# Optimization experiments

Measured on AMD Instinct MI355X. Metric: run time of the kernel, lower is better.

Reference implementation:

```python
import jax, jax.numpy as jnp
import numpy as np

B, N, M, F = 64, 2048, 2048, 4   # batch, n_pred_points, n_gt_points, feature cols
D = 2                            # loss_indices = [0, 1] -> (x, y) coords


def setup_inputs() -> dict:
    key = jax.random.key(0)
    k1, k2 = jax.random.split(key)
    preds = jax.random.normal(k1, (B, N, F), dtype=jnp.float32)
    targs = jax.random.normal(k2, (B, M, F), dtype=jnp.float32)
    subcoef = jnp.ones((D,), dtype=jnp.float32)
    return {"preds": preds, "targs": targs, "subcoef": subcoef}


def _bidirectional_nn_loss(p, t, subcoef):
    # p: [B, N, D] pred coords, t: [B, M, D] gt coords
    # squared euclidean pairwise distances [B, N, M]
    d2 = (jnp.sum(p * p, axis=-1)[:, :, None]
          + jnp.sum(t * t, axis=-1)[:, None, :]
          - 2.0 * jnp.einsum('bnd,bmd->bnm', p, t))
    # gt_tree: nearest gt for every pred point
    nn_gt = jnp.argmin(d2, axis=2)    # [B, N]
    # pred_tree: nearest pred for every gt point
    nn_pr = jnp.argmin(d2, axis=1)    # [B, M]
    t_nn = jnp.take_along_axis(t, nn_gt[:, :, None], axis=1)  # [B, N, D]
    p_nn = jnp.take_along_axis(p, nn_pr[:, :, None], axis=1)  # [B, M, D]
    move_preds_to_gt = jnp.sum(jnp.abs(p - t_nn) * subcoef)   # subcoef only on this term
    move_gts_to_pred = jnp.sum(jnp.abs(p_nn - t))
    return move_preds_to_gt + move_gts_to_pred


def reference(preds, targs, subcoef):
    p = preds[..., :D]   # loss_indices = [0, 1]
    t = targs[..., :D]
    return _bidirectional_nn_loss(p, t, subcoef)
```

## Files before the change

kernel.cpp:

```cpp
#include <hip/hip_runtime.h>

constexpr int B = 64;
constexpr int NQ = 2048;
constexpr int M = 2048;
constexpr int F = 4;
constexpr int BLOCK = 256;
constexpr int P = 8;
constexpr int CHUNK = 16;
constexpr int NCHUNK = M / CHUNK;
constexpr unsigned DMASK = 0xFFFFFF80u;
constexpr float BIAS = 64.0f;
constexpr int QTOT = 2 * B * NQ;
constexpr int QHALF = QTOT / 2;

typedef float v2f __attribute__((ext_vector_type(2)));

__device__ __forceinline__ unsigned fbits(float x) {
    union { float f; unsigned u; } c; c.f = x; return c.u;
}
__device__ __forceinline__ float min3f(float a, float b, float c) {
    float r;
    asm("v_min3_f32 %0, %1, %2, %3" : "=v"(r) : "v"(a), "v"(b), "v"(c));
    return r;
}

template <int S>
__global__ void __launch_bounds__(BLOCK)
nn_scan(const float* __restrict__ preds,
        const float* __restrict__ targs,
        unsigned* __restrict__ keys,
        float* __restrict__ out) {
    constexpr int CPB = NCHUNK / S;
    __shared__ float4 sxy[CPB * 8];
    __shared__ float2 snm[CPB * 8];

    const int s   = blockIdx.x;
    const int b   = blockIdx.y;
    const int dir = blockIdx.z;
    const int tid = threadIdx.x;

    if (s == 0 && b == 0 && dir == 0 && tid == 0) *out = 0.0f;

    const float* qsrc = dir ? targs : preds;
    const float* csrc = dir ? preds : targs;

    const float* cb_ = csrc + ((size_t)b * M + (size_t)s * CPB * CHUNK) * F;
    for (int g = tid; g < CPB * 8; g += BLOCK) {
        const float4 a = *reinterpret_cast<const float4*>(cb_ + (size_t)(2 * g) * F);
        const float4 c = *reinterpret_cast<const float4*>(cb_ + (size_t)(2 * g + 1) * F);
        sxy[g] = make_float4(a.x, c.x, a.y, c.y);
        snm[g] = make_float2(fmaf(a.y, a.y, a.x * a.x) + BIAS,
                             fmaf(c.y, c.y, c.x * c.x) + BIAS);
    }
    __syncthreads();

    float ax[P], ay[P];
    unsigned bkey[P];
    #pragma unroll
    for (int j = 0; j < P; ++j) {
        const int n = j * BLOCK + tid;
        const float2 p = *reinterpret_cast<const float2*>(qsrc + ((size_t)b * NQ + n) * F);
        ax[j] = -2.0f * p.x;
        ay[j] = -2.0f * p.y;
        bkey[j] = 0xFFFFFFFFu;
    }

    #pragma unroll 2
    for (int c = 0; c < CPB; ++c) {
        float cbm[P];
        #pragma unroll
        for (int j = 0; j < P; ++j) cbm[j] = 3.4028235e38f;
        #pragma unroll
        for (int i = 0; i < 8; ++i) {
            const float4 q  = sxy[c * 8 + i];
            const float2 nn = snm[c * 8 + i];
            #pragma unroll
            for (int j = 0; j < P; ++j) {
                const float d0 = fmaf(ax[j], q.x, fmaf(ay[j], q.z, nn.x));
                const float d1 = fmaf(ax[j], q.y, fmaf(ay[j], q.w, nn.y));
                cbm[j] = min3f(d0, d1, cbm[j]);
            }
        }
        const unsigned gc = (unsigned)(s * CPB + c);
        #pragma unroll
        for (int j = 0; j < P; ++j) {
            const unsigned key = (fbits(cbm[j]) & DMASK) | gc;
            bkey[j] = key < bkey[j] ? key : bkey[j];
        }
    }

    unsigned* kout = keys + (size_t)s * QTOT + ((size_t)dir * B + b) * NQ;
    #pragma unroll
    for (int j = 0; j < P; ++j) kout[j * BLOCK + tid] = bkey[j];
}

template <int S>
__global__ void __launch_bounds__(BLOCK)
nn_combine(const float* __restrict__ preds,
           const float* __restrict__ targs,
           const float* __restrict__ subcoef,
           const unsigned* __restrict__ keys,
           float* __restrict__ out) {
    __shared__ float wsum[BLOCK / 64];
    const int q0 = blockIdx.x * BLOCK + threadIdx.x;
    const int b  = q0 >> 11;
    const int n  = q0 & 2047;

    const float c0 = subcoef[0], c1 = subcoef[1];
    float acc = 0.0f;

    #pragma unroll
    for (int dir = 0; dir < 2; ++dir) {
        const int qid = q0 + dir * QHALF;
        const float* qsrc = dir ? targs : preds;
        const float* csrc = dir ? preds : targs;
        const float2 p = *reinterpret_cast<const float2*>(qsrc + ((size_t)b * NQ + n) * F);
        const float ax = -2.0f * p.x, ay = -2.0f * p.y;

        unsigned k = 0xFFFFFFFFu;
        #pragma unroll
        for (int s = 0; s < S; ++s) {
            const unsigned ks = keys[(size_t)s * QTOT + qid];
            k = ks < k ? ks : k;
        }
        const int cwin = (int)(k & 0x7Fu);
        const unsigned dbits = k & DMASK;

        const float4* cand = reinterpret_cast<const float4*>(
            csrc + ((size_t)b * M + (size_t)cwin * CHUNK) * F);
        float qx = 0.0f, qy = 0.0f;
        int found = 0;
        #pragma unroll
        for (int i = 0; i < CHUNK; ++i) {
            const float4 t4 = cand[i];
            const float x = t4.x, y = t4.y;
            const float nrm = fmaf(y, y, x * x) + BIAS;
            const float d = fmaf(ax, x, fmaf(ay, y, nrm));
            const bool hit = (((fbits(d) & DMASK) == dbits) && !found);
            qx = hit ? x : qx;
            qy = hit ? y : qy;
            found = hit ? 1 : found;
        }
        if (!found) { qx = cand[0].x; qy = cand[0].y; }

        const float w0 = dir ? 1.0f : c0;
        const float w1 = dir ? 1.0f : c1;
        acc += fabsf(p.x - qx) * w0 + fabsf(p.y - qy) * w1;
    }

    #pragma unroll
    for (int off = 32; off > 0; off >>= 1) acc += __shfl_down(acc, off, 64);
    if ((threadIdx.x & 63) == 0) wsum[threadIdx.x >> 6] = acc;
    __syncthreads();
    if (threadIdx.x == 0) {
        float ssum = 0.0f;
        #pragma unroll
        for (int w = 0; w < BLOCK / 64; ++w) ssum += wsum[w];
        atomicAdd(out, ssum);
    }
}

constexpr int PF = 2;
constexpr int CH_F4 = 9;
__global__ void __launch_bounds__(BLOCK)
nn_fallback(const float* __restrict__ preds,
            const float* __restrict__ targs,
            const float* __restrict__ subcoef,
            float* __restrict__ out) {
    __shared__ float4 sc4[NCHUNK * CH_F4];
    __shared__ float  wsum[BLOCK / 64];
    const int dir = blockIdx.z, b = blockIdx.y, tid = threadIdx.x;
    const float* src = dir ? targs : preds;
    const float* dst = dir ? preds : targs;
    const float* dstb = dst + (size_t)b * M * F;
    for (int g = tid; g < M / 2; g += BLOCK) {
        const float4 a = *reinterpret_cast<const float4*>(dstb + (size_t)(2 * g) * F);
        const float4 c = *reinterpret_cast<const float4*>(dstb + (size_t)(2 * g + 1) * F);
        sc4[(g >> 3) * CH_F4 + (g & 7)] = make_float4(a.x, c.x, a.y, c.y);
    }
    __syncthreads();
    const int base = blockIdx.x * (BLOCK * PF);
    float px[PF], py[PF], axr[PF], ayr[PF];
    unsigned bkey[PF];
    #pragma unroll
    for (int j = 0; j < PF; ++j) {
        const int n = base + j * BLOCK + tid;
        const float2 p = *reinterpret_cast<const float2*>(src + ((size_t)b * NQ + n) * F);
        px[j] = p.x; py[j] = p.y;
        axr[j] = -2.0f * p.x; ayr[j] = -2.0f * p.y;
        bkey[j] = 0xFFFFFFFFu;
    }
    for (int c = 0; c < NCHUNK; ++c) {
        const float4* chp = sc4 + c * CH_F4;
        float cbm[PF];
        #pragma unroll
        for (int j = 0; j < PF; ++j) cbm[j] = 3.4028235e38f;
        #pragma unroll
        for (int i = 0; i < CHUNK / 2; ++i) {
            const float4 q = chp[i];
            const float n0 = fmaf(q.z, q.z, q.x * q.x) + BIAS;
            const float n1 = fmaf(q.w, q.w, q.y * q.y) + BIAS;
            #pragma unroll
            for (int j = 0; j < PF; ++j) {
                const float d0 = fmaf(axr[j], q.x, fmaf(ayr[j], q.z, n0));
                const float d1 = fmaf(axr[j], q.y, fmaf(ayr[j], q.w, n1));
                cbm[j] = min3f(d0, d1, cbm[j]);
            }
        }
        #pragma unroll
        for (int j = 0; j < PF; ++j) {
            const unsigned key = (fbits(cbm[j]) & DMASK) | (unsigned)c;
            bkey[j] = key < bkey[j] ? key : bkey[j];
        }
    }
    float c0 = 1.0f, c1 = 1.0f;
    if (dir == 0) { c0 = subcoef[0]; c1 = subcoef[1]; }
    float acc = 0.0f;
    #pragma unroll
    for (int j = 0; j < PF; ++j) {
        const int cwin = (int)(bkey[j] & 0x7Fu);
        const unsigned dbits = bkey[j] & DMASK;
        const float4* chp = sc4 + cwin * CH_F4;
        float qx = 0.0f, qy = 0.0f; int found = 0;
        #pragma unroll
        for (int i = 0; i < CHUNK / 2; ++i) {
            const float4 q = chp[i];
            const float n0 = fmaf(q.z, q.z, q.x * q.x) + BIAS;
            const float dA = fmaf(axr[j], q.x, fmaf(ayr[j], q.z, n0));
            bool hit = (((fbits(dA) & DMASK) == dbits) && !found);
            qx = hit ? q.x : qx; qy = hit ? q.z : qy; found = hit ? 1 : found;
            const float n1 = fmaf(q.w, q.w, q.y * q.y) + BIAS;
            const float dB = fmaf(axr[j], q.y, fmaf(ayr[j], q.w, n1));
            hit = (((fbits(dB) & DMASK) == dbits) && !found);
            qx = hit ? q.y : qx; qy = hit ? q.w : qy; found = hit ? 1 : found;
        }
        acc += fabsf(px[j] - qx) * c0 + fabsf(py[j] - qy) * c1;
    }
    #pragma unroll
    for (int off = 32; off > 0; off >>= 1) acc += __shfl_down(acc, off, 64);
    if ((tid & 63) == 0) wsum[tid >> 6] = acc;
    __syncthreads();
    if (tid == 0) {
        float ssum = 0.0f;
        #pragma unroll
        for (int w = 0; w < BLOCK / 64; ++w) ssum += wsum[w];
        atomicAdd(out, ssum);
    }
}

extern "C" void kernel_launch(void* const* d_in, const int* in_sizes, int n_in,
                              void* d_out, int out_size, void* d_ws, size_t ws_size,
                              hipStream_t stream) {
    const float* preds   = (const float*)d_in[0];
    const float* targs   = (const float*)d_in[1];
    const float* subcoef = (const float*)d_in[2];
    float* out = (float*)d_out;

    const size_t need16 = (size_t)16 * QTOT * sizeof(unsigned);
    const size_t need8  = (size_t)8  * QTOT * sizeof(unsigned);
    const size_t need4  = (size_t)4  * QTOT * sizeof(unsigned);

    if (d_ws != nullptr && ws_size >= need4) {
        unsigned* keys = (unsigned*)d_ws;
        if (ws_size >= need16) {
            nn_scan<16><<<dim3(16, B, 2), BLOCK, 0, stream>>>(preds, targs, keys, out);
            nn_combine<16><<<dim3(QHALF / BLOCK), BLOCK, 0, stream>>>(preds, targs, subcoef, keys, out);
        } else if (ws_size >= need8) {
            nn_scan<8><<<dim3(8, B, 2), BLOCK, 0, stream>>>(preds, targs, keys, out);
            nn_combine<8><<<dim3(QHALF / BLOCK), BLOCK, 0, stream>>>(preds, targs, subcoef, keys, out);
        } else {
            nn_scan<4><<<dim3(4, B, 2), BLOCK, 0, stream>>>(preds, targs, keys, out);
            nn_combine<4><<<dim3(QHALF / BLOCK), BLOCK, 0, stream>>>(preds, targs, subcoef, keys, out);
        }
    } else {
        hipMemsetAsync(out, 0, sizeof(float), stream);
        dim3 grid(NQ / (BLOCK * PF), B, 2);
        nn_fallback<<<grid, BLOCK, 0, stream>>>(preds, targs, subcoef, out);
    }
}
```

Baseline: 109.3 us.

## Stage candidate coordinates in LDS for combine kernel and regrid per batch/direction

The combine kernel now runs one block per (quarter, batch, direction). Each block first loads the batch's candidate points into shared memory in the same interleaved x/y layout the scan uses. The rematch pass over the winning 16-point chunk then reads from LDS instead of doing scattered 16-byte global loads per query. This trades redundant staging (each block loads the whole 2048-point set for only 512 queries) and an extra barrier for removing random global gathers.

```diff
diff --git a/kernel.cpp b/kernel.cpp
--- a/kernel.cpp
+++ b/kernel.cpp
@@ -8,12 +8,11 @@
 constexpr int P = 8;
 constexpr int CHUNK = 16;
 constexpr int NCHUNK = M / CHUNK;
+constexpr int CH_F4 = 9;
 constexpr unsigned DMASK = 0xFFFFFF80u;
 constexpr float BIAS = 64.0f;
 constexpr int QTOT = 2 * B * NQ;
 constexpr int QHALF = QTOT / 2;
-
-typedef float v2f __attribute__((ext_vector_type(2)));
 
 __device__ __forceinline__ unsigned fbits(float x) {
     union { float f; unsigned u; } c; c.f = x; return c.u;
@@ -101,58 +100,71 @@
            const float* __restrict__ subcoef,
            const unsigned* __restrict__ keys,
            float* __restrict__ out) {
-    __shared__ float wsum[BLOCK / 64];
-    const int q0 = blockIdx.x * BLOCK + threadIdx.x;
-    const int b  = q0 >> 11;
-    const int n  = q0 & 2047;
-
-    const float c0 = subcoef[0], c1 = subcoef[1];
+    __shared__ float4 sc4[NCHUNK * CH_F4];
+    __shared__ float  wsum[BLOCK / 64];
+
+    const int quad = blockIdx.x;
+    const int b    = blockIdx.y;
+    const int dir  = blockIdx.z;
+    const int tid  = threadIdx.x;
+
+    const float* qsrc = dir ? targs : preds;
+    const float* csrc = dir ? preds : targs;
+
+    const float* cbase = csrc + (size_t)b * M * F;
+    for (int g = tid; g < M / 2; g += BLOCK) {
+        const float4 a = *reinterpret_cast<const float4*>(cbase + (size_t)(2 * g) * F);
+        const float4 c = *reinterpret_cast<const float4*>(cbase + (size_t)(2 * g + 1) * F);
+        sc4[(g >> 3) * CH_F4 + (g & 7)] = make_float4(a.x, c.x, a.y, c.y);
+    }
+    __syncthreads();
+
+    const float w0 = dir ? 1.0f : subcoef[0];
+    const float w1 = dir ? 1.0f : subcoef[1];
     float acc = 0.0f;
 
     #pragma unroll
-    for (int dir = 0; dir < 2; ++dir) {
-        const int qid = q0 + dir * QHALF;
-        const float* qsrc = dir ? targs : preds;
-        const float* csrc = dir ? preds : targs;
+    for (int j = 0; j < 2; ++j) {
+        const int n   = quad * 512 + j * BLOCK + tid;
+        const int qid = dir * QHALF + b * NQ + n;
         const float2 p = *reinterpret_cast<const float2*>(qsrc + ((size_t)b * NQ + n) * F);
         const float ax = -2.0f * p.x, ay = -2.0f * p.y;
 
         unsigned k = 0xFFFFFFFFu;
+        const unsigned* kp = keys + qid;
         #pragma unroll
         for (int s = 0; s < S; ++s) {
-            const unsigned ks = keys[(size_t)s * QTOT + qid];
+            const unsigned ks = kp[(size_t)s * QTOT];
             k = ks < k ? ks : k;
         }
         const int cwin = (int)(k & 0x7Fu);
         const unsigned dbits = k & DMASK;
 
-        const float4* cand = reinterpret_cast<const float4*>(
-            csrc + ((size_t)b * M + (size_t)cwin * CHUNK) * F);
+        const float4* chp = sc4 + cwin * CH_F4;
         float qx = 0.0f, qy = 0.0f;
         int found = 0;
         #pragma unroll
-        for (int i = 0; i < CHUNK; ++i) {
-            const float4 t4 = cand[i];
-            const float x = t4.x, y = t4.y;
-            const float nrm = fmaf(y, y, x * x) + BIAS;
-            const float d = fmaf(ax, x, fmaf(ay, y, nrm));
-            const bool hit = (((fbits(d) & DMASK) == dbits) && !found);
-            qx = hit ? x : qx;
-            qy = hit ? y : qy;
-            found = hit ? 1 : found;
-        }
-        if (!found) { qx = cand[0].x; qy = cand[0].y; }
-
-        const float w0 = dir ? 1.0f : c0;
-        const float w1 = dir ? 1.0f : c1;
+        for (int i = 0; i < 8; ++i) {
+            const float4 q = chp[i];
+            const float n0 = fmaf(q.z, q.z, q.x * q.x) + BIAS;
+            const float d0 = fmaf(ax, q.x, fmaf(ay, q.z, n0));
+            bool hit = (((fbits(d0) & DMASK) == dbits) && !found);
+            qx = hit ? q.x : qx;  qy = hit ? q.z : qy;  found = hit ? 1 : found;
+            const float n1 = fmaf(q.w, q.w, q.y * q.y) + BIAS;
+            const float d1 = fmaf(ax, q.y, fmaf(ay, q.w, n1));
+            hit = (((fbits(d1) & DMASK) == dbits) && !found);
+            qx = hit ? q.y : qx;  qy = hit ? q.w : qy;  found = hit ? 1 : found;
+        }
+        if (!found) { qx = sc4[cwin * CH_F4].x; qy = sc4[cwin * CH_F4].z; }
+
         acc += fabsf(p.x - qx) * w0 + fabsf(p.y - qy) * w1;
     }
 
     #pragma unroll
     for (int off = 32; off > 0; off >>= 1) acc += __shfl_down(acc, off, 64);
-    if ((threadIdx.x & 63) == 0) wsum[threadIdx.x >> 6] = acc;
-    __syncthreads();
-    if (threadIdx.x == 0) {
+    if ((tid & 63) == 0) wsum[tid >> 6] = acc;
+    __syncthreads();
+    if (tid == 0) {
         float ssum = 0.0f;
         #pragma unroll
         for (int w = 0; w < BLOCK / 64; ++w) ssum += wsum[w];
@@ -161,7 +173,6 @@
 }
 
 constexpr int PF = 2;
-constexpr int CH_F4 = 9;
 __global__ void __launch_bounds__(BLOCK)
 nn_fallback(const float* __restrict__ preds,
             const float* __restrict__ targs,
@@ -264,13 +275,13 @@
         unsigned* keys = (unsigned*)d_ws;
         if (ws_size >= need16) {
             nn_scan<16><<<dim3(16, B, 2), BLOCK, 0, stream>>>(preds, targs, keys, out);
-            nn_combine<16><<<dim3(QHALF / BLOCK), BLOCK, 0, stream>>>(preds, targs, subcoef, keys, out);
+            nn_combine<16><<<dim3(4, B, 2), BLOCK, 0, stream>>>(preds, targs, subcoef, keys, out);
         } else if (ws_size >= need8) {
             nn_scan<8><<<dim3(8, B, 2), BLOCK, 0, stream>>>(preds, targs, keys, out);
-            nn_combine<8><<<dim3(QHALF / BLOCK), BLOCK, 0, stream>>>(preds, targs, subcoef, keys, out);
+            nn_combine<8><<<dim3(4, B, 2), BLOCK, 0, stream>>>(preds, targs, subcoef, keys, out);
         } else {
             nn_scan<4><<<dim3(4, B, 2), BLOCK, 0, stream>>>(preds, targs, keys, out);
-            nn_combine<4><<<dim3(QHALF / BLOCK), BLOCK, 0, stream>>>(preds, targs, subcoef, keys, out);
+            nn_combine<4><<<dim3(4, B, 2), BLOCK, 0, stream>>>(preds, targs, subcoef, keys, out);
         }
     } else {
         hipMemsetAsync(out, 0, sizeof(float), stream);
```

New measurement: 107.9 us. About the same (-1.3%).
